# Performance work log

Hardware: AMD Instinct MI355X
Metric: run time of the kernel (lower is better)

The kernel has to match this reference:

```python
import math
import jax, jax.numpy as jnp
import numpy as np

E = 24  # num experts


def layer_norm(x, w, b, eps=1e-6):
    m = x.mean(-1, keepdims=True)
    v = x.var(-1, keepdims=True)
    return (x - m) / jnp.sqrt(v + eps) * w + b


def top2_dispatch(x, Wg, C):
    # x: [S, d] -> combine/dispatch: [S, E, C] (GShard/DeepSpeed top-2 gating)
    logits = x @ Wg                                   # [S, E]
    gates = jax.nn.softmax(logits, axis=-1)
    idx1 = jnp.argmax(gates, axis=-1)
    m1 = jax.nn.one_hot(idx1, E, dtype=x.dtype)       # [S, E]
    masked = jnp.where(m1 > 0, -jnp.inf, logits)
    idx2 = jnp.argmax(masked, axis=-1)
    m2 = jax.nn.one_hot(idx2, E, dtype=x.dtype)
    # position of each token within its expert's capacity buffer
    loc1 = jnp.cumsum(m1, axis=0) - m1
    loc2 = jnp.cumsum(m2, axis=0) - m2 + jnp.sum(m1, axis=0, keepdims=True)
    m1 = m1 * (loc1 < C)                              # drop overflow tokens
    m2 = m2 * (loc2 < C)
    g1 = jnp.sum(gates * m1, axis=-1)
    g2 = jnp.sum(gates * m2, axis=-1)
    denom = jnp.maximum(g1 + g2, 1e-9)
    g1, g2 = g1 / denom, g2 / denom
    p1 = jnp.sum(loc1 * m1, axis=-1).astype(jnp.int32)
    p2 = jnp.sum(loc2 * m2, axis=-1).astype(jnp.int32)
    c1 = g1[:, None, None] * m1[:, :, None] * jax.nn.one_hot(p1, C, dtype=x.dtype)[:, None, :]
    c2 = g2[:, None, None] * m2[:, :, None] * jax.nn.one_hot(p2, C, dtype=x.dtype)[:, None, :]
    combine = c1 + c2                                  # [S, E, C]
    dispatch = (combine > 0).astype(x.dtype)
    return combine, dispatch


def moe_apply(x, combine, dispatch, W, b):
    # dispatch tokens to expert buffers, per-expert GEMM, combine back
    disp = jnp.einsum('sec,sd->ecd', dispatch, x)      # [E, C, d]
    h = jnp.einsum('ecd,edf->ecf', disp, W) + b[:, None, :]
    return jnp.einsum('sec,ecf->sf', combine, h)       # [S, f]


def setup_inputs() -> dict:
    b, seq, d_in, d_hid = 4, 2048, 1024, 4096
    ks = jax.random.split(jax.random.key(0), 6)
    s = 0.02
    return {
        'x': jax.random.normal(ks[0], (b, seq, d_in), dtype=jnp.float32),
        'Wg': jax.random.normal(ks[1], (d_in, E), dtype=jnp.float32) * s,
        'W1': jax.random.normal(ks[2], (E, d_in, d_hid), dtype=jnp.float32) * s,
        'b1': jnp.zeros((E, d_hid), dtype=jnp.float32),
        'W2': jax.random.normal(ks[3], (E, d_hid, d_in), dtype=jnp.float32) * s,
        'b2': jnp.zeros((E, d_in), dtype=jnp.float32),
        'ln_hid_w': jnp.ones((4, d_hid), dtype=jnp.float32),
        'ln_hid_b': jnp.zeros((4, d_hid), dtype=jnp.float32),
        'ln_out_w': jnp.ones((d_in,), dtype=jnp.float32),
        'ln_out_b': jnp.zeros((d_in,), dtype=jnp.float32),
    }


def reference(x, Wg, W1, b1, W2, b2, ln_hid_w, ln_hid_b, ln_out_w, ln_out_b):
    bsz, seq, d = x.shape
    H = 4
    n = seq // H
    S = bsz * n  # tokens per sub-sequence MoE call
    C = math.ceil(2 * S / E)  # top-2 capacity, capacity_factor=1.0
    # b (h n) c -> h (b n) c
    xg = x.reshape(bsz, H, n, d).transpose(1, 0, 2, 3).reshape(H, S, d)

    def per_group(xf, lw, lb):
        combine, dispatch = top2_dispatch(xf, Wg, C)
        h = moe_apply(xf, combine, dispatch, W1, b1)       # [S, d_hid]
        h = layer_norm(h, lw, lb)
        h = jax.nn.relu(h)                                  # dropout = identity (eval)
        return moe_apply(h, combine, dispatch, W2, b2)      # reuse gate_decision

    out = jax.vmap(per_group)(xg, ln_hid_w, ln_hid_b)       # [H, S, d]
    out = out.reshape(H, bsz, n, d).transpose(1, 0, 2, 3).reshape(bsz, seq, d)
    return layer_norm(out + x, ln_out_w, ln_out_b)
```

## Files before the change

kernel.cpp:

```cpp
#include <hip/hip_runtime.h>
#include <cstdint>
#include <cstddef>

#define E_      24
#define D_IN    1024
#define D_HID   4096
#define HGRP    4
#define BSZ     4
#define SEQ     2048
#define NSUB    512
#define S_      2048
#define NTOKG   8192
#define CAP     171
#define MR      768
#define MTILE   3

typedef __attribute__((ext_vector_type(4))) float          f32x4;
typedef __attribute__((ext_vector_type(2))) float          f32x2;
typedef __attribute__((ext_vector_type(4))) unsigned short u16x4;
typedef __attribute__((ext_vector_type(8))) unsigned short u16x8;
typedef __attribute__((ext_vector_type(4))) unsigned int   u32x4;
typedef __attribute__((ext_vector_type(8))) short          s16x8;

__device__ __forceinline__ unsigned short f2bf(float f) {
  unsigned int u = __float_as_uint(f);
  u += 0x7fffu + ((u >> 16) & 1u);
  return (unsigned short)(u >> 16);
}
__device__ __forceinline__ float bf2f(unsigned short v) {
  return __uint_as_float(((unsigned int)v) << 16);
}

__global__ __launch_bounds__(64)
void k_gating(const float* __restrict__ x, const float* __restrict__ Wg,
              int* __restrict__ tokE1, int* __restrict__ tokE2,
              float* __restrict__ tokG1, float* __restrict__ tokG2) {
  int tg = blockIdx.x;
  int h = tg >> 11, s = tg & 2047;
  int bi = s >> 9, ni = s & 511;
  const float* xr = x + ((size_t)bi*SEQ + (size_t)h*NSUB + ni) * D_IN;
  int lane = threadIdx.x;
  float acc[E_];
  #pragma unroll
  for (int e = 0; e < E_; ++e) acc[e] = 0.f;
  #pragma unroll
  for (int it = 0; it < D_IN/256; ++it) {
    f32x4 xv = *(const f32x4*)(xr + it*256 + lane*4);
    #pragma unroll
    for (int j = 0; j < 4; ++j) {
      float xs = xv[j];
      const float* wrow = Wg + (size_t)(it*256 + lane*4 + j) * E_;
      #pragma unroll
      for (int e = 0; e < E_; ++e) acc[e] += xs * wrow[e];
    }
  }
  #pragma unroll
  for (int e = 0; e < E_; ++e) {
    float v = acc[e];
    v += __shfl_xor(v, 32); v += __shfl_xor(v, 16); v += __shfl_xor(v, 8);
    v += __shfl_xor(v, 4);  v += __shfl_xor(v, 2);  v += __shfl_xor(v, 1);
    acc[e] = v;
  }
  if (lane == 0) {
    float mx = acc[0];
    #pragma unroll
    for (int e = 1; e < E_; ++e) mx = fmaxf(mx, acc[e]);
    float den = 0.f;
    #pragma unroll
    for (int e = 0; e < E_; ++e) den += expf(acc[e] - mx);
    int i1 = 0; float v1 = acc[0];
    #pragma unroll
    for (int e = 1; e < E_; ++e) if (acc[e] > v1) { v1 = acc[e]; i1 = e; }
    int i2 = -1; float v2 = -3.4e38f;
    #pragma unroll
    for (int e = 0; e < E_; ++e) if (e != i1 && acc[e] > v2) { v2 = acc[e]; i2 = e; }
    tokE1[tg] = i1; tokE2[tg] = i2;
    tokG1[tg] = expf(v1 - mx) / den;
    tokG2[tg] = expf(v2 - mx) / den;
  }
}

__global__ void k_init_slots(int* __restrict__ slotTok) {
  slotTok[blockIdx.x*256 + threadIdx.x] = -1;
}

__global__ __launch_bounds__(64)
void k_scan(const int* __restrict__ tokE1, const int* __restrict__ tokE2,
            float* __restrict__ tokG1, float* __restrict__ tokG2,
            int* __restrict__ tokP1, int* __restrict__ tokP2,
            int* __restrict__ slotTok) {
  int h = blockIdx.x;
  int lane = threadIdx.x;
  __shared__ int cnt[64][E_];
  __shared__ int tot1[E_];
  const int CH = S_/64;
  const int* e1 = tokE1 + h*S_;
  const int* e2 = tokE2 + h*S_;
  #pragma unroll
  for (int e = 0; e < E_; ++e) cnt[lane][e] = 0;
  __syncthreads();
  for (int k = 0; k < CH; ++k) cnt[lane][e1[lane*CH + k]]++;
  __syncthreads();
  if (lane < E_) {
    int run = 0;
    for (int j = 0; j < 64; ++j) { int t = cnt[j][lane]; cnt[j][lane] = run; run += t; }
    tot1[lane] = run;
  }
  __syncthreads();
  for (int k = 0; k < CH; ++k) {
    int s = lane*CH + k;
    int e = e1[s];
    int p = cnt[lane][e]++;
    int tg = h*S_ + s;
    if (p < CAP) { tokP1[tg] = p; slotTok[e*MR + h*CAP + p] = tg; }
    else         { tokP1[tg] = -1; }
  }
  __syncthreads();
  #pragma unroll
  for (int e = 0; e < E_; ++e) cnt[lane][e] = 0;
  __syncthreads();
  for (int k = 0; k < CH; ++k) cnt[lane][e2[lane*CH + k]]++;
  __syncthreads();
  if (lane < E_) {
    int run = tot1[lane];
    for (int j = 0; j < 64; ++j) { int t = cnt[j][lane]; cnt[j][lane] = run; run += t; }
  }
  __syncthreads();
  for (int k = 0; k < CH; ++k) {
    int s = lane*CH + k;
    int e = e2[s];
    int p = cnt[lane][e]++;
    int tg = h*S_ + s;
    if (p < CAP) { tokP2[tg] = p; slotTok[e*MR + h*CAP + p] = tg; }
    else         { tokP2[tg] = -1; }
  }
  __syncthreads();
  for (int k = 0; k < CH; ++k) {
    int tg = h*S_ + k*64 + lane;
    float g1 = (tokP1[tg] >= 0) ? tokG1[tg] : 0.f;
    float g2 = (tokP2[tg] >= 0) ? tokG2[tg] : 0.f;
    float den = fmaxf(g1 + g2, 1e-9f);
    tokG1[tg] = g1 / den;
    tokG2[tg] = g2 / den;
  }
}

__global__ __launch_bounds__(256)
void k_gather1(const float* __restrict__ x, const int* __restrict__ slotTok,
               unsigned short* __restrict__ A1) {
  int row = blockIdx.x;
  int tok = slotTok[row];
  int t = threadIdx.x;
  int k = t*4;
  int ba = ((k & 63)*2) ^ ((row & 7) << 4);
  char* dst = (char*)A1 + (size_t)row*(D_IN*2) + (size_t)(k >> 6)*128 + ba;
  u16x4 pk;
  if (tok >= 0) {
    int h = tok >> 11, s = tok & 2047;
    int bi = s >> 9, ni = s & 511;
    const float* xr = x + ((size_t)bi*SEQ + (size_t)h*NSUB + ni) * D_IN;
    f32x4 v = *(const f32x4*)(xr + k);
    pk.x = f2bf(v.x); pk.y = f2bf(v.y); pk.z = f2bf(v.z); pk.w = f2bf(v.w);
  } else {
    pk.x = 0; pk.y = 0; pk.z = 0; pk.w = 0;
  }
  *(u16x4*)dst = pk;
}

template<int K, int N>
__global__ __launch_bounds__(512, 2)
void k_gemm(const unsigned short* __restrict__ A, const float* __restrict__ W,
            const float* __restrict__ bias, unsigned short* __restrict__ Out) {
  const int NT = N / 256;
  int cpx = gridDim.x >> 3;
  int lb = blockIdx.x;
  int bid = (lb & 7) * cpx + (lb >> 3);
  int mt  = bid % MTILE;
  int rem = bid / MTILE;
  int nt  = rem % NT;
  int e   = rem / NT;

  const char*  Ab = (const char*)A + ((size_t)e*MR + (size_t)mt*256) * (K*2);
  const float* We = W + (size_t)e*K*N + (size_t)nt*256;

  __shared__ unsigned short As0[256*64];
  __shared__ unsigned short As1[256*64];
  __shared__ unsigned short Bs0[256*64];
  __shared__ unsigned short Bs1[256*64];

  int tid  = threadIdx.x;
  int lane = tid & 63;
  int wid  = tid >> 6;
  int wr = wid >> 2, wc = wid & 3;

  f32x4 acc[8][4];
  #pragma unroll
  for (int i = 0; i < 8; ++i)
    #pragma unroll
    for (int j = 0; j < 4; ++j) acc[i][j] = (f32x4)0.f;

  int cB  = tid & 127;
  int bkh = (tid >> 7) * 16;
  float w0[16], w1[16];

  auto loadB = [&](int kt) {
    const float* p = We + (size_t)(kt*64 + bkh)*N + cB;
    #pragma unroll
    for (int q = 0; q < 16; ++q) { w0[q] = p[(size_t)q*N]; w1[q] = p[(size_t)q*N + 128]; }
  };
  auto storeB = [&](unsigned short* Bs) {
    #pragma unroll
    for (int h = 0; h < 2; ++h) {
      u16x8 c0, c1;
      #pragma unroll
      for (int q = 0; q < 8; ++q) { c0[q] = f2bf(w0[h*8+q]); c1[q] = f2bf(w1[h*8+q]); }
      int kbb = bkh*2 + 16*h;
      int n0 = cB, n1 = cB + 128;
      *(u16x8*)((char*)Bs + n0*128 + (kbb ^ ((n0 & 7) << 4))) = c0;
      *(u16x8*)((char*)Bs + n1*128 + (kbb ^ ((n1 & 7) << 4))) = c1;
    }
  };
  auto stageA = [&](int kt, int half, unsigned short* As) {
    #pragma unroll
    for (int i = 0; i < 2; ++i) {
      int L = i*8192 + tid*16;
      const char* src = Ab + (size_t)(half*128 + (L >> 7))*(K*2) + (size_t)kt*128 + (L & 127);
      __builtin_amdgcn_global_load_lds(
          (const __attribute__((address_space(1))) void*)src,
          (__attribute__((address_space(3))) void*)((char*)As + half*16384 + L),
          16, 0, 0);
    }
  };
  auto dsFrags = [&](const unsigned short* As, const unsigned short* Bs,
                     int ra, int ks, s16x8* afr, s16x8* bfr) {
    int kb = ks*64 + (lane >> 4)*16;
    #pragma unroll
    for (int i = 0; i < 4; ++i) {
      int r = wr*128 + ra*64 + i*16 + (lane & 15);
      afr[i] = *(const s16x8*)((const char*)As + r*128 + (kb ^ ((r & 7) << 4)));
      int c = wc*64 + i*16 + (lane & 15);
      bfr[i] = *(const s16x8*)((const char*)Bs + c*128 + (kb ^ ((c & 7) << 4)));
    }
  };
  auto mfmaQ = [&](int ra, const s16x8* afr, const s16x8* bfr) {
    __builtin_amdgcn_s_setprio(1);
    #pragma unroll
    for (int i = 0; i < 4; ++i)
      #pragma unroll
      for (int j = 0; j < 4; ++j)
        acc[ra*4+i][j] = __builtin_amdgcn_mfma_f32_16x16x32_bf16(afr[i], bfr[j], acc[ra*4+i][j], 0, 0, 0);
    __builtin_amdgcn_s_setprio(0);
  };

  unsigned short *Acur = As0, *Anxt = As1, *Bcur = Bs0, *Bnxt = Bs1;
  const int NKT = K / 64;

  stageA(0, 0, Acur); stageA(0, 1, Acur);
  loadB(0);
  storeB(Bcur);
  asm volatile("s_waitcnt vmcnt(0)" ::: "memory");
  __syncthreads();

  for (int kt = 0; kt < NKT; ++kt) {
    int ktn = (kt + 1 < NKT) ? kt + 1 : NKT - 1;
    s16x8 afr[4], bfr[4];
    dsFrags(Acur, Bcur, 0, 0, afr, bfr);
    stageA(ktn, 0, Anxt);
    __builtin_amdgcn_s_barrier();
    mfmaQ(0, afr, bfr);
    dsFrags(Acur, Bcur, 1, 0, afr, bfr);
    loadB(ktn);
    __builtin_amdgcn_sched_barrier(0);
    __builtin_amdgcn_s_barrier();
    mfmaQ(1, afr, bfr);
    dsFrags(Acur, Bcur, 0, 1, afr, bfr);
    stageA(ktn, 1, Anxt);
    __builtin_amdgcn_s_barrier();
    mfmaQ(0, afr, bfr);
    dsFrags(Acur, Bcur, 1, 1, afr, bfr);
    __builtin_amdgcn_s_barrier();
    mfmaQ(1, afr, bfr);
    storeB(Bnxt);
    asm volatile("s_waitcnt vmcnt(0)" ::: "memory");
    __syncthreads();
    unsigned short* t1 = Acur; Acur = Anxt; Anxt = t1;
    unsigned short* t2 = Bcur; Bcur = Bnxt; Bnxt = t2;
  }

  #pragma unroll
  for (int j = 0; j < 4; ++j) {
    int col = nt*256 + wc*64 + j*16 + (lane & 15);
    float bv = bias[(size_t)e*N + col];
    #pragma unroll
    for (int i = 0; i < 8; ++i) {
      int rowb = mt*256 + wr*128 + i*16 + (lane >> 4)*4;
      #pragma unroll
      for (int r = 0; r < 4; ++r) {
        float v = acc[i][j][r] + bv;
        Out[(size_t)e*MR*N + (size_t)(rowb + r)*N + col] = f2bf(v);
      }
    }
  }
}

__global__ __launch_bounds__(256)
void k_zero_empty(const int* __restrict__ slotTok, unsigned short* __restrict__ A2) {
  int row = blockIdx.x;
  if (slotTok[row] >= 0) return;
  u32x4 z = (u32x4)0u;
  char* base = (char*)A2 + (size_t)row*(D_HID*2) + threadIdx.x*32;
  *(u32x4*)base = z;
  *(u32x4*)(base + 16) = z;
}

__global__ __launch_bounds__(256)
void k_combine_ln(const unsigned short* __restrict__ H1,
                  const int* __restrict__ tokE1, const int* __restrict__ tokE2,
                  const int* __restrict__ tokP1, const int* __restrict__ tokP2,
                  const float* __restrict__ tokG1, const float* __restrict__ tokG2,
                  const float* __restrict__ lnw, const float* __restrict__ lnb,
                  unsigned short* __restrict__ A2) {
  int tg = blockIdx.x;
  int h = tg >> 11;
  int p1 = tokP1[tg], p2 = tokP2[tg];
  if (p1 < 0 && p2 < 0) return;
  float g1 = tokG1[tg], g2 = tokG2[tg];
  long r1 = (p1 >= 0) ? ((long)tokE1[tg]*MR + h*CAP + p1) : -1;
  long r2 = (p2 >= 0) ? ((long)tokE2[tg]*MR + h*CAP + p2) : -1;
  int t = threadIdx.x;
  float v[16];
  float sum = 0.f, sq = 0.f;
  #pragma unroll
  for (int u = 0; u < 4; ++u) {
    int f = u*1024 + t*4;
    float a0 = 0.f, a1 = 0.f, a2 = 0.f, a3 = 0.f;
    if (r1 >= 0) {
      u16x4 q = *(const u16x4*)(H1 + (size_t)r1*D_HID + f);
      a0 += g1*bf2f(q.x); a1 += g1*bf2f(q.y); a2 += g1*bf2f(q.z); a3 += g1*bf2f(q.w);
    }
    if (r2 >= 0) {
      u16x4 q = *(const u16x4*)(H1 + (size_t)r2*D_HID + f);
      a0 += g2*bf2f(q.x); a1 += g2*bf2f(q.y); a2 += g2*bf2f(q.z); a3 += g2*bf2f(q.w);
    }
    v[u*4+0] = a0; v[u*4+1] = a1; v[u*4+2] = a2; v[u*4+3] = a3;
    sum += a0 + a1 + a2 + a3;
    sq  += a0*a0 + a1*a1 + a2*a2 + a3*a3;
  }
  #pragma unroll
  for (int o = 32; o; o >>= 1) { sum += __shfl_xor(sum, o); sq += __shfl_xor(sq, o); }
  __shared__ float redA[4], redB[4];
  int wid = t >> 6;
  if ((t & 63) == 0) { redA[wid] = sum; redB[wid] = sq; }
  __syncthreads();
  float S = redA[0] + redA[1] + redA[2] + redA[3];
  float Q = redB[0] + redB[1] + redB[2] + redB[3];
  float m = S * (1.f / D_HID);
  float var = Q * (1.f / D_HID) - m*m;
  float rs = rsqrtf(var + 1e-6f);
  #pragma unroll
  for (int u = 0; u < 4; ++u) {
    int f = u*1024 + t*4;
    u16x4 pk;
    float y0 = fmaxf((v[u*4+0]-m)*rs*lnw[h*D_HID+f+0] + lnb[h*D_HID+f+0], 0.f);
    float y1 = fmaxf((v[u*4+1]-m)*rs*lnw[h*D_HID+f+1] + lnb[h*D_HID+f+1], 0.f);
    float y2 = fmaxf((v[u*4+2]-m)*rs*lnw[h*D_HID+f+2] + lnb[h*D_HID+f+2], 0.f);
    float y3 = fmaxf((v[u*4+3]-m)*rs*lnw[h*D_HID+f+3] + lnb[h*D_HID+f+3], 0.f);
    pk.x = f2bf(y0); pk.y = f2bf(y1); pk.z = f2bf(y2); pk.w = f2bf(y3);
    int chunk = f >> 6;
    int ob = (f & 63)*2;
    if (r1 >= 0)
      *(u16x4*)((char*)A2 + (size_t)r1*(D_HID*2) + (size_t)chunk*128 + (ob ^ (((int)r1 & 7) << 4))) = pk;
    if (r2 >= 0)
      *(u16x4*)((char*)A2 + (size_t)r2*(D_HID*2) + (size_t)chunk*128 + (ob ^ (((int)r2 & 7) << 4))) = pk;
  }
}

__global__ __launch_bounds__(256)
void k_final(const unsigned short* __restrict__ H2, const float* __restrict__ x,
             const int* __restrict__ tokE1, const int* __restrict__ tokE2,
             const int* __restrict__ tokP1, const int* __restrict__ tokP2,
             const float* __restrict__ tokG1, const float* __restrict__ tokG2,
             const float* __restrict__ lnw, const float* __restrict__ lnb,
             float* __restrict__ out) {
  int tg = blockIdx.x;
  int h = tg >> 11, s = tg & 2047;
  int bi = s >> 9, ni = s & 511;
  size_t xoff = ((size_t)bi*SEQ + (size_t)h*NSUB + ni) * D_IN;
  int p1 = tokP1[tg], p2 = tokP2[tg];
  float g1 = tokG1[tg], g2 = tokG2[tg];
  int t = threadIdx.x;
  int f = t*4;
  f32x4 xv = *(const f32x4*)(x + xoff + f);
  float v0 = xv.x, v1 = xv.y, v2 = xv.z, v3 = xv.w;
  if (p1 >= 0) {
    size_t r1 = (size_t)tokE1[tg]*MR + h*CAP + p1;
    u16x4 q = *(const u16x4*)(H2 + r1*D_IN + f);
    v0 += g1*bf2f(q.x); v1 += g1*bf2f(q.y); v2 += g1*bf2f(q.z); v3 += g1*bf2f(q.w);
  }
  if (p2 >= 0) {
    size_t r2 = (size_t)tokE2[tg]*MR + h*CAP + p2;
    u16x4 q = *(const u16x4*)(H2 + r2*D_IN + f);
    v0 += g2*bf2f(q.x); v1 += g2*bf2f(q.y); v2 += g2*bf2f(q.z); v3 += g2*bf2f(q.w);
  }
  float sum = v0+v1+v2+v3, sq = v0*v0+v1*v1+v2*v2+v3*v3;
  #pragma unroll
  for (int o = 32; o; o >>= 1) { sum += __shfl_xor(sum, o); sq += __shfl_xor(sq, o); }
  __shared__ float redA[4], redB[4];
  int wid = t >> 6;
  if ((t & 63) == 0) { redA[wid] = sum; redB[wid] = sq; }
  __syncthreads();
  float S = redA[0] + redA[1] + redA[2] + redA[3];
  float Q = redB[0] + redB[1] + redB[2] + redB[3];
  float m = S * (1.f / D_IN);
  float var = Q * (1.f / D_IN) - m*m;
  float rs = rsqrtf(var + 1e-6f);
  f32x4 res;
  res.x = (v0 - m)*rs*lnw[f+0] + lnb[f+0];
  res.y = (v1 - m)*rs*lnw[f+1] + lnb[f+1];
  res.z = (v2 - m)*rs*lnw[f+2] + lnb[f+2];
  res.w = (v3 - m)*rs*lnw[f+3] + lnb[f+3];
  *(f32x4*)(out + xoff + f) = res;
}

extern "C" void kernel_launch(void* const* d_in, const int* in_sizes, int n_in,
                              void* d_out, int out_size, void* d_ws, size_t ws_size,
                              hipStream_t stream) {
  const float* x    = (const float*)d_in[0];
  const float* Wg   = (const float*)d_in[1];
  const float* W1   = (const float*)d_in[2];
  const float* b1   = (const float*)d_in[3];
  const float* W2   = (const float*)d_in[4];
  const float* b2   = (const float*)d_in[5];
  const float* lnhw = (const float*)d_in[6];
  const float* lnhb = (const float*)d_in[7];
  const float* lnow = (const float*)d_in[8];
  const float* lnob = (const float*)d_in[9];
  float* out = (float*)d_out;
  (void)in_sizes; (void)n_in; (void)out_size; (void)ws_size;

  char* ws = (char*)d_ws;
  size_t off = 0;
  auto take = [&](size_t bytes) -> char* {
    char* p = ws + off;
    off += (bytes + 255) & ~(size_t)255;
    return p;
  };
  int*   tokE1 = (int*)take(NTOKG*sizeof(int));
  int*   tokE2 = (int*)take(NTOKG*sizeof(int));
  int*   tokP1 = (int*)take(NTOKG*sizeof(int));
  int*   tokP2 = (int*)take(NTOKG*sizeof(int));
  float* tokG1 = (float*)take(NTOKG*sizeof(float));
  float* tokG2 = (float*)take(NTOKG*sizeof(float));
  int*   slotTok = (int*)take((size_t)E_*MR*sizeof(int));
  unsigned short* A1 = (unsigned short*)take((size_t)E_*MR*D_IN*2);
  unsigned short* H1 = (unsigned short*)take((size_t)E_*MR*D_HID*2);
  unsigned short* A2 = (unsigned short*)take((size_t)E_*MR*D_HID*2);
  unsigned short* H2 = (unsigned short*)take((size_t)E_*MR*D_IN*2);

  k_init_slots<<<dim3(E_*MR/256), dim3(256), 0, stream>>>(slotTok);
  k_gating<<<dim3(NTOKG), dim3(64), 0, stream>>>(x, Wg, tokE1, tokE2, tokG1, tokG2);
  k_scan<<<dim3(HGRP), dim3(64), 0, stream>>>(tokE1, tokE2, tokG1, tokG2, tokP1, tokP2, slotTok);
  k_gather1<<<dim3(E_*MR), dim3(256), 0, stream>>>(x, slotTok, A1);
  k_gemm<D_IN, D_HID><<<dim3(E_*(D_HID/256)*MTILE), dim3(512), 0, stream>>>(A1, W1, b1, H1);
  k_zero_empty<<<dim3(E_*MR), dim3(256), 0, stream>>>(slotTok, A2);
  k_combine_ln<<<dim3(NTOKG), dim3(256), 0, stream>>>(H1, tokE1, tokE2, tokP1, tokP2,
                                                      tokG1, tokG2, lnhw, lnhb, A2);
  k_gemm<D_HID, D_IN><<<dim3(E_*(D_IN/256)*MTILE), dim3(512), 0, stream>>>(A2, W2, b2, H2);
  k_final<<<dim3(NTOKG), dim3(256), 0, stream>>>(H2, x, tokE1, tokE2, tokP1, tokP2,
                                                 tokG1, tokG2, lnow, lnob, out);
}
```

Baseline: 855.1 us.

## Pre-convert weights to swizzled bf16 and split-K the second expert GEMM

Adds a kernel that transposes and converts the fp32 expert weights into a pre-swizzled bf16 N-major buffer. Both GEMMs can then stage A and B straight into LDS with async global_load_lds instead of converting B in registers. The second GEMM is split four ways along K to put more blocks on the device, writing bf16 partials into the reused H1 buffer, and k_final sums them. This costs an extra full pass over the weights each call, one more bf16 rounding of the partials, and more traffic in k_final.

```diff
diff --git a/kernel.cpp b/kernel.cpp
--- a/kernel.cpp
+++ b/kernel.cpp
@@ -14,9 +14,9 @@
 #define CAP     171
 #define MR      768
 #define MTILE   3
+#define KSPL2   4
 
 typedef __attribute__((ext_vector_type(4))) float          f32x4;
-typedef __attribute__((ext_vector_type(2))) float          f32x2;
 typedef __attribute__((ext_vector_type(4))) unsigned short u16x4;
 typedef __attribute__((ext_vector_type(8))) unsigned short u16x8;
 typedef __attribute__((ext_vector_type(4))) unsigned int   u32x4;
@@ -168,20 +168,64 @@
 }
 
 template<int K, int N>
+__global__ __launch_bounds__(256)
+void k_cvtW(const float* __restrict__ W, unsigned short* __restrict__ Wt) {
+  const int NB = N/64, KB = K/64;
+  int bid = blockIdx.x;
+  int kb = bid % KB;
+  int rem = bid / KB;
+  int nb = rem % NB;
+  int e  = rem / NB;
+  __shared__ float lds[64][65];
+  int t = threadIdx.x;
+  int kl = t >> 2, ng = (t & 3) * 16;
+  const float* src = W + ((size_t)e*K + (size_t)kb*64 + kl)*N + (size_t)nb*64 + ng;
+  f32x4 v0 = *(const f32x4*)(src);
+  f32x4 v1 = *(const f32x4*)(src + 4);
+  f32x4 v2 = *(const f32x4*)(src + 8);
+  f32x4 v3 = *(const f32x4*)(src + 12);
+  #pragma unroll
+  for (int j = 0; j < 4; ++j) lds[ng +  0 + j][kl] = v0[j];
+  #pragma unroll
+  for (int j = 0; j < 4; ++j) lds[ng +  4 + j][kl] = v1[j];
+  #pragma unroll
+  for (int j = 0; j < 4; ++j) lds[ng +  8 + j][kl] = v2[j];
+  #pragma unroll
+  for (int j = 0; j < 4; ++j) lds[ng + 12 + j][kl] = v3[j];
+  __syncthreads();
+  int nl = t >> 2, kg = (t & 3) * 16;
+  u16x8 c0, c1;
+  #pragma unroll
+  for (int j = 0; j < 8; ++j) {
+    c0[j] = f2bf(lds[nl][kg + j]);
+    c1[j] = f2bf(lds[nl][kg + 8 + j]);
+  }
+  char* dst = (char*)Wt + ((size_t)e*N + (size_t)nb*64 + nl)*(K*2) + (size_t)kb*128;
+  int sw = (nl & 7) << 4;
+  *(u16x8*)(dst + ((kg*2)      ^ sw)) = c0;
+  *(u16x8*)(dst + ((kg*2 + 16) ^ sw)) = c1;
+}
+
+template<int KROW, int KCHUNK, int N>
 __global__ __launch_bounds__(512, 2)
-void k_gemm(const unsigned short* __restrict__ A, const float* __restrict__ W,
+void k_gemm(const unsigned short* __restrict__ A, const unsigned short* __restrict__ Wt,
             const float* __restrict__ bias, unsigned short* __restrict__ Out) {
   const int NT = N / 256;
+  const int KSPLIT = KROW / KCHUNK;
+  const int NKT = KCHUNK / 64;
   int cpx = gridDim.x >> 3;
   int lb = blockIdx.x;
   int bid = (lb & 7) * cpx + (lb >> 3);
   int mt  = bid % MTILE;
   int rem = bid / MTILE;
+  int kc  = rem % KSPLIT;
+  rem /= KSPLIT;
   int nt  = rem % NT;
   int e   = rem / NT;
 
-  const char*  Ab = (const char*)A + ((size_t)e*MR + (size_t)mt*256) * (K*2);
-  const float* We = W + (size_t)e*K*N + (size_t)nt*256;
+  const char* Ab = (const char*)A  + ((size_t)e*MR + (size_t)mt*256) * (KROW*2);
+  const char* Bb = (const char*)Wt + ((size_t)e*N  + (size_t)nt*256) * (KROW*2);
+  size_t kbase = (size_t)kc * (KCHUNK*2);
 
   __shared__ unsigned short As0[256*64];
   __shared__ unsigned short As1[256*64];
@@ -199,50 +243,40 @@
     #pragma unroll
     for (int j = 0; j < 4; ++j) acc[i][j] = (f32x4)0.f;
 
-  int cB  = tid & 127;
-  int bkh = (tid >> 7) * 16;
-  float w0[16], w1[16];
-
-  auto loadB = [&](int kt) {
-    const float* p = We + (size_t)(kt*64 + bkh)*N + cB;
-    #pragma unroll
-    for (int q = 0; q < 16; ++q) { w0[q] = p[(size_t)q*N]; w1[q] = p[(size_t)q*N + 128]; }
+  auto stage = [&](int kt2, unsigned short* As, unsigned short* Bs) {
+    size_t koff = kbase + (size_t)kt2*128;
+    #pragma unroll
+    for (int i = 0; i < 4; ++i) {
+      int L = i*8192 + tid*16;
+      __builtin_amdgcn_global_load_lds(
+          (const __attribute__((address_space(1))) void*)(Ab + (size_t)(L >> 7)*(KROW*2) + koff + (L & 127)),
+          (__attribute__((address_space(3))) void*)((char*)As + L), 16, 0, 0);
+    }
+    #pragma unroll
+    for (int i = 0; i < 4; ++i) {
+      int L = i*8192 + tid*16;
+      __builtin_amdgcn_global_load_lds(
+          (const __attribute__((address_space(1))) void*)(Bb + (size_t)(L >> 7)*(KROW*2) + koff + (L & 127)),
+          (__attribute__((address_space(3))) void*)((char*)Bs + L), 16, 0, 0);
+    }
   };
-  auto storeB = [&](unsigned short* Bs) {
-    #pragma unroll
-    for (int h = 0; h < 2; ++h) {
-      u16x8 c0, c1;
-      #pragma unroll
-      for (int q = 0; q < 8; ++q) { c0[q] = f2bf(w0[h*8+q]); c1[q] = f2bf(w1[h*8+q]); }
-      int kbb = bkh*2 + 16*h;
-      int n0 = cB, n1 = cB + 128;
-      *(u16x8*)((char*)Bs + n0*128 + (kbb ^ ((n0 & 7) << 4))) = c0;
-      *(u16x8*)((char*)Bs + n1*128 + (kbb ^ ((n1 & 7) << 4))) = c1;
-    }
-  };
-  auto stageA = [&](int kt, int half, unsigned short* As) {
-    #pragma unroll
-    for (int i = 0; i < 2; ++i) {
-      int L = i*8192 + tid*16;
-      const char* src = Ab + (size_t)(half*128 + (L >> 7))*(K*2) + (size_t)kt*128 + (L & 127);
-      __builtin_amdgcn_global_load_lds(
-          (const __attribute__((address_space(1))) void*)src,
-          (__attribute__((address_space(3))) void*)((char*)As + half*16384 + L),
-          16, 0, 0);
-    }
-  };
-  auto dsFrags = [&](const unsigned short* As, const unsigned short* Bs,
-                     int ra, int ks, s16x8* afr, s16x8* bfr) {
+  auto fragsA = [&](const unsigned short* As, int ra, int ks, s16x8* afr) {
     int kb = ks*64 + (lane >> 4)*16;
     #pragma unroll
     for (int i = 0; i < 4; ++i) {
       int r = wr*128 + ra*64 + i*16 + (lane & 15);
       afr[i] = *(const s16x8*)((const char*)As + r*128 + (kb ^ ((r & 7) << 4)));
-      int c = wc*64 + i*16 + (lane & 15);
-      bfr[i] = *(const s16x8*)((const char*)Bs + c*128 + (kb ^ ((c & 7) << 4)));
     }
   };
-  auto mfmaQ = [&](int ra, const s16x8* afr, const s16x8* bfr) {
+  auto fragsB = [&](const unsigned short* Bs, int ks, s16x8* bfr) {
+    int kb = ks*64 + (lane >> 4)*16;
+    #pragma unroll
+    for (int j = 0; j < 4; ++j) {
+      int c = wc*64 + j*16 + (lane & 15);
+      bfr[j] = *(const s16x8*)((const char*)Bs + c*128 + (kb ^ ((c & 7) << 4)));
+    }
+  };
+  auto mfma16 = [&](int ra, const s16x8* afr, const s16x8* bfr) {
     __builtin_amdgcn_s_setprio(1);
     #pragma unroll
     for (int i = 0; i < 4; ++i)
@@ -252,52 +286,56 @@
     __builtin_amdgcn_s_setprio(0);
   };
 
-  unsigned short *Acur = As0, *Anxt = As1, *Bcur = Bs0, *Bnxt = Bs1;
-  const int NKT = K / 64;
-
-  stageA(0, 0, Acur); stageA(0, 1, Acur);
-  loadB(0);
-  storeB(Bcur);
-  asm volatile("s_waitcnt vmcnt(0)" ::: "memory");
-  __syncthreads();
-
-  for (int kt = 0; kt < NKT; ++kt) {
-    int ktn = (kt + 1 < NKT) ? kt + 1 : NKT - 1;
+  auto tile = [&](int t, const unsigned short* Ac, const unsigned short* Bc,
+                  unsigned short* An, unsigned short* Bn) {
+    int tn = (t + 1 < NKT) ? t + 1 : t;
     s16x8 afr[4], bfr[4];
-    dsFrags(Acur, Bcur, 0, 0, afr, bfr);
-    stageA(ktn, 0, Anxt);
-    __builtin_amdgcn_s_barrier();
-    mfmaQ(0, afr, bfr);
-    dsFrags(Acur, Bcur, 1, 0, afr, bfr);
-    loadB(ktn);
+    stage(tn, An, Bn);
+    fragsA(Ac, 0, 0, afr); fragsB(Bc, 0, bfr);
+    __builtin_amdgcn_s_barrier();
+    asm volatile("s_waitcnt lgkmcnt(0)" ::: "memory");
     __builtin_amdgcn_sched_barrier(0);
-    __builtin_amdgcn_s_barrier();
-    mfmaQ(1, afr, bfr);
-    dsFrags(Acur, Bcur, 0, 1, afr, bfr);
-    stageA(ktn, 1, Anxt);
-    __builtin_amdgcn_s_barrier();
-    mfmaQ(0, afr, bfr);
-    dsFrags(Acur, Bcur, 1, 1, afr, bfr);
-    __builtin_amdgcn_s_barrier();
-    mfmaQ(1, afr, bfr);
-    storeB(Bnxt);
-    asm volatile("s_waitcnt vmcnt(0)" ::: "memory");
+    mfma16(0, afr, bfr);
+    __builtin_amdgcn_s_barrier();
+    fragsA(Ac, 1, 0, afr);
+    __builtin_amdgcn_s_barrier();
+    asm volatile("s_waitcnt lgkmcnt(0)" ::: "memory");
+    __builtin_amdgcn_sched_barrier(0);
+    mfma16(1, afr, bfr);
+    __builtin_amdgcn_s_barrier();
+    fragsA(Ac, 0, 1, afr); fragsB(Bc, 1, bfr);
+    __builtin_amdgcn_s_barrier();
+    asm volatile("s_waitcnt lgkmcnt(0)" ::: "memory");
+    __builtin_amdgcn_sched_barrier(0);
+    mfma16(0, afr, bfr);
+    __builtin_amdgcn_s_barrier();
+    fragsA(Ac, 1, 1, afr);
+    __builtin_amdgcn_s_barrier();
+    asm volatile("s_waitcnt lgkmcnt(0)" ::: "memory");
+    __builtin_amdgcn_sched_barrier(0);
+    mfma16(1, afr, bfr);
     __syncthreads();
-    unsigned short* t1 = Acur; Acur = Anxt; Anxt = t1;
-    unsigned short* t2 = Bcur; Bcur = Bnxt; Bnxt = t2;
-  }
-
+  };
+
+  stage(0, As0, Bs0);
+  __syncthreads();
+  for (int kt = 0; kt < NKT; kt += 2) {
+    tile(kt,     As0, Bs0, As1, Bs1);
+    tile(kt + 1, As1, Bs1, As0, Bs0);
+  }
+
+  unsigned short* Op = Out + (size_t)kc * ((size_t)E_*MR*N);
   #pragma unroll
   for (int j = 0; j < 4; ++j) {
     int col = nt*256 + wc*64 + j*16 + (lane & 15);
-    float bv = bias[(size_t)e*N + col];
+    float bv = (kc == 0) ? bias[(size_t)e*N + col] : 0.f;
     #pragma unroll
     for (int i = 0; i < 8; ++i) {
       int rowb = mt*256 + wr*128 + i*16 + (lane >> 4)*4;
       #pragma unroll
       for (int r = 0; r < 4; ++r) {
         float v = acc[i][j][r] + bv;
-        Out[(size_t)e*MR*N + (size_t)(rowb + r)*N + col] = f2bf(v);
+        Op[(size_t)e*MR*N + (size_t)(rowb + r)*N + col] = f2bf(v);
       }
     }
   }
@@ -376,12 +414,13 @@
 }
 
 __global__ __launch_bounds__(256)
-void k_final(const unsigned short* __restrict__ H2, const float* __restrict__ x,
+void k_final(const unsigned short* __restrict__ H2p, const float* __restrict__ x,
              const int* __restrict__ tokE1, const int* __restrict__ tokE2,
              const int* __restrict__ tokP1, const int* __restrict__ tokP2,
              const float* __restrict__ tokG1, const float* __restrict__ tokG2,
              const float* __restrict__ lnw, const float* __restrict__ lnb,
              float* __restrict__ out) {
+  const size_t PSTR = (size_t)E_*MR*D_IN;
   int tg = blockIdx.x;
   int h = tg >> 11, s = tg & 2047;
   int bi = s >> 9, ni = s & 511;
@@ -394,13 +433,23 @@
   float v0 = xv.x, v1 = xv.y, v2 = xv.z, v3 = xv.w;
   if (p1 >= 0) {
     size_t r1 = (size_t)tokE1[tg]*MR + h*CAP + p1;
-    u16x4 q = *(const u16x4*)(H2 + r1*D_IN + f);
-    v0 += g1*bf2f(q.x); v1 += g1*bf2f(q.y); v2 += g1*bf2f(q.z); v3 += g1*bf2f(q.w);
+    float a0 = 0.f, a1 = 0.f, a2 = 0.f, a3 = 0.f;
+    #pragma unroll
+    for (int p = 0; p < KSPL2; ++p) {
+      u16x4 q = *(const u16x4*)(H2p + p*PSTR + r1*D_IN + f);
+      a0 += bf2f(q.x); a1 += bf2f(q.y); a2 += bf2f(q.z); a3 += bf2f(q.w);
+    }
+    v0 += g1*a0; v1 += g1*a1; v2 += g1*a2; v3 += g1*a3;
   }
   if (p2 >= 0) {
     size_t r2 = (size_t)tokE2[tg]*MR + h*CAP + p2;
-    u16x4 q = *(const u16x4*)(H2 + r2*D_IN + f);
-    v0 += g2*bf2f(q.x); v1 += g2*bf2f(q.y); v2 += g2*bf2f(q.z); v3 += g2*bf2f(q.w);
+    float a0 = 0.f, a1 = 0.f, a2 = 0.f, a3 = 0.f;
+    #pragma unroll
+    for (int p = 0; p < KSPL2; ++p) {
+      u16x4 q = *(const u16x4*)(H2p + p*PSTR + r2*D_IN + f);
+      a0 += bf2f(q.x); a1 += bf2f(q.y); a2 += bf2f(q.z); a3 += bf2f(q.w);
+    }
+    v0 += g2*a0; v1 += g2*a1; v2 += g2*a2; v3 += g2*a3;
   }
   float sum = v0+v1+v2+v3, sq = v0*v0+v1*v1+v2*v2+v3*v3;
   #pragma unroll
@@ -455,17 +504,20 @@
   unsigned short* A1 = (unsigned short*)take((size_t)E_*MR*D_IN*2);
   unsigned short* H1 = (unsigned short*)take((size_t)E_*MR*D_HID*2);
   unsigned short* A2 = (unsigned short*)take((size_t)E_*MR*D_HID*2);
-  unsigned short* H2 = (unsigned short*)take((size_t)E_*MR*D_IN*2);
+  unsigned short* Wt = (unsigned short*)take((size_t)E_*D_IN*D_HID*2);
+  unsigned short* H2p = H1;
 
   k_init_slots<<<dim3(E_*MR/256), dim3(256), 0, stream>>>(slotTok);
   k_gating<<<dim3(NTOKG), dim3(64), 0, stream>>>(x, Wg, tokE1, tokE2, tokG1, tokG2);
   k_scan<<<dim3(HGRP), dim3(64), 0, stream>>>(tokE1, tokE2, tokG1, tokG2, tokP1, tokP2, slotTok);
   k_gather1<<<dim3(E_*MR), dim3(256), 0, stream>>>(x, slotTok, A1);
-  k_gemm<D_IN, D_HID><<<dim3(E_*(D_HID/256)*MTILE), dim3(512), 0, stream>>>(A1, W1, b1, H1);
+  k_cvtW<D_IN, D_HID><<<dim3(E_*(D_HID/64)*(D_IN/64)), dim3(256), 0, stream>>>(W1, Wt);
+  k_gemm<D_IN, D_IN, D_HID><<<dim3(E_*(D_HID/256)*MTILE), dim3(512), 0, stream>>>(A1, Wt, b1, H1);
   k_zero_empty<<<dim3(E_*MR), dim3(256), 0, stream>>>(slotTok, A2);
   k_combine_ln<<<dim3(NTOKG), dim3(256), 0, stream>>>(H1, tokE1, tokE2, tokP1, tokP2,
                                                       tokG1, tokG2, lnhw, lnhb, A2);
-  k_gemm<D_HID, D_IN><<<dim3(E_*(D_IN/256)*MTILE), dim3(512), 0, stream>>>(A2, W2, b2, H2);
-  k_final<<<dim3(NTOKG), dim3(256), 0, stream>>>(H2, x, tokE1, tokE2, tokP1, tokP2,
+  k_cvtW<D_HID, D_IN><<<dim3(E_*(D_IN/64)*(D_HID/64)), dim3(256), 0, stream>>>(W2, Wt);
+  k_gemm<D_HID, D_IN, D_IN><<<dim3(E_*(D_IN/256)*MTILE*KSPL2), dim3(512), 0, stream>>>(A2, Wt, b2, H2p);
+  k_final<<<dim3(NTOKG), dim3(256), 0, stream>>>(H2p, x, tokE1, tokE2, tokP1, tokP2,
                                                  tokG1, tokG2, lnow, lnob, out);
 }
```

Result: slower. 898.1 us (+5.0%).
